# Kernel optimization log

Measured on AMD Instinct MI355X. Metric: run time of the kernel, lower is better.

The kernel has to match this reference:

```python
import jax, jax.numpy as jnp
import numpy as np

POS_MARGIN = 0.1
NEG_MARGIN = 1.4
LOG_SCALE = 24.0
MAX_POINTS = 256

N_FULL = 50000
M_C = 2048
N_C = 2048
D_FEAT = 256
K_CORR = 4096
N_BACK = 30000


def setup_inputs() -> dict:
    key = jax.random.key(0)
    ks = jax.random.split(key, 12)
    ref_feats = jax.random.normal(ks[4], (M_C, D_FEAT), jnp.float32)
    src_feats = jax.random.normal(ks[5], (N_C, D_FEAT), jnp.float32)
    # features are assumed L2-normalized (pairwise_distance(..., normalized=True))
    ref_feats = ref_feats / jnp.linalg.norm(ref_feats, axis=-1, keepdims=True)
    src_feats = src_feats / jnp.linalg.norm(src_feats, axis=-1, keepdims=True)
    return {
        "ref_points": jax.random.normal(ks[0], (N_FULL, 3), jnp.float32),
        "src_points": jax.random.normal(ks[1], (N_FULL, 3), jnp.float32),
        "ref_points_c": jax.random.normal(ks[2], (M_C, 3), jnp.float32),
        "src_points_c": jax.random.normal(ks[3], (N_C, 3), jnp.float32),
        "ref_feats_c": ref_feats,
        "src_feats_c": src_feats,
        "gt_node_corr_indices": jax.random.randint(ks[6], (K_CORR, 2), 0, M_C, dtype=jnp.int64) if jax.config.jax_enable_x64 else jax.random.randint(ks[6], (K_CORR, 2), 0, M_C, dtype=jnp.int32),
        "gt_node_corr_overlaps": jax.random.uniform(ks[7], (K_CORR,), jnp.float32),
        "corr_sp_mask": jax.random.uniform(ks[8], (M_C + N_C,), jnp.float32),
        "ref_back_indices": jax.random.randint(ks[9], (N_BACK,), 0, N_FULL, dtype=jnp.int32),
        "src_back_indices": jax.random.randint(ks[10], (N_BACK,), 0, N_FULL, dtype=jnp.int32),
    }


def _nn_indices(full_points, corr_points):
    # argmin over squared euclidean distance == argmin over cdist(p=2)
    d = (jnp.sum(corr_points ** 2, axis=1)[:, None]
         + jnp.sum(full_points ** 2, axis=1)[None, :]
         - 2.0 * corr_points @ full_points.T)  # [k, N]
    return jnp.argmin(d, axis=1)


def _forward(ref_points, src_points, ref_points_c, src_points_c,
             ref_feats_c, src_feats_c, gt_node_corr_overlaps, corr_sp_mask,
             gt_node_corr_indices, ref_back_indices, src_back_indices):
    m = ref_feats_c.shape[0]
    n = src_feats_c.shape[0]

    idx_ref = _nn_indices(ref_points, ref_points_c)  # [m]
    idx_src = _nn_indices(src_points, src_points_c)  # [n]

    # mask_ref[i] True iff idx_ref[i] appears in ref_back_indices (set intersection semantics)
    mask_ref = jnp.any(idx_ref[:, None] == ref_back_indices[None, :], axis=1)
    mask_src = jnp.any(idx_src[:, None] == src_back_indices[None, :], axis=1)

    xi = gt_node_corr_indices[:, 0]
    yi = gt_node_corr_indices[:, 1]
    corr_gt = jnp.zeros((m, n), dtype=bool).at[xi, yi].set(True)
    corr_overlap = jnp.zeros((m, n), jnp.float32).at[xi, yi].set(gt_node_corr_overlaps)

    corr_gt = corr_gt & (mask_ref[:, None] & mask_src[None, :])
    gt_mask = jnp.concatenate([mask_ref, mask_src]).astype(jnp.float32)  # [m+n]

    # cap number of positives at MAX_POINTS by overlap score
    count = jnp.sum(corr_gt)
    score = jnp.where(corr_gt, corr_overlap, -1.0).reshape(-1)
    topv, topi = jax.lax.top_k(score, MAX_POINTS)
    capped = jnp.zeros((m * n,), dtype=bool).at[topi].set(topv > -0.5).reshape(m, n)
    corr_gt = jnp.where(count > MAX_POINTS, capped, corr_gt)

    var_mask = 1.0 - corr_sp_mask  # [m+n]

    # NLLLaplace
    feat_sq = jnp.maximum(2.0 - 2.0 * (ref_feats_c @ src_feats_c.T), 0.0)
    feat_dists = jnp.sqrt(feat_sq)  # [m, n]
    laplace_mask = var_mask[:m][:, None] * var_mask[m:m + n][None, :]
    feat_dists = jnp.exp(0.5 * laplace_mask) * feat_dists

    not_pos = (~corr_gt).astype(jnp.float32)
    not_neg = corr_gt.astype(jnp.float32)
    pos_w = jax.lax.stop_gradient(
        jnp.maximum(feat_dists - 100000.0 * not_pos - POS_MARGIN, 0.0))
    neg_w = jax.lax.stop_gradient(
        jnp.maximum(NEG_MARGIN - (feat_dists + 100000.0 * not_neg), 0.0))

    lp = LOG_SCALE * (feat_dists - POS_MARGIN) * pos_w
    ln = LOG_SCALE * (NEG_MARGIN - feat_dists) * neg_w
    loss_row = jax.nn.softplus(jax.nn.logsumexp(lp, axis=-1) + jax.nn.logsumexp(ln, axis=-1)) / LOG_SCALE
    loss_col = jax.nn.softplus(jax.nn.logsumexp(lp, axis=-2) + jax.nn.logsumexp(ln, axis=-2)) / LOG_SCALE
    loss1 = (jnp.mean(loss_row) + jnp.mean(loss_col)) / 2.0
    loss2 = jnp.mean(jnp.abs(var_mask - gt_mask))
    loss = loss1 + loss2
    return loss, loss1, loss2


def reference(ref_points, src_points, ref_points_c, src_points_c,
              ref_feats_c, src_feats_c, gt_node_corr_indices,
              gt_node_corr_overlaps, corr_sp_mask,
              ref_back_indices, src_back_indices):
    return _forward(ref_points, src_points, ref_points_c, src_points_c,
                    ref_feats_c, src_feats_c, gt_node_corr_overlaps, corr_sp_mask,
                    gt_node_corr_indices, ref_back_indices, src_back_indices)
```

## Files before the change

kernel.cpp:

```cpp
#include <hip/hip_runtime.h>
#include <math.h>

using u8  = unsigned char;
using u32 = unsigned int;
using u64 = unsigned long long;

typedef short short8 __attribute__((ext_vector_type(8)));
typedef float f32x4  __attribute__((ext_vector_type(4)));

#define MC 2048
#define NC 2048
#define DF 256
#define NFULL 50000
#define NBACK 30000
#define KCORR 4096
#define MAXPTS 256
#define NN_CHUNK 196
#define BM_WORDS_I 1568

constexpr size_t OFF_ROWP = 0;
constexpr size_t OFF_COLP = (size_t)2 * 1024 * 1024;
constexpr size_t OFF_GTB  = (size_t)3 * 1024 * 1024;
constexpr size_t OFF_NN   = OFF_GTB + (size_t)512 * 1024;
constexpr size_t OFF_CAND = OFF_NN + 4096 * 8;
constexpr size_t OFF_ACC  = OFF_CAND + 4096 * 8;
constexpr size_t OFF_CNT  = OFF_ACC + 256;
constexpr size_t OFF_BM   = OFF_CNT + 256;
constexpr size_t OFF_HASH = OFF_BM + 3200 * 4;

__global__ __launch_bounds__(256) void k_init(uint4* __restrict__ gtb4, u64* __restrict__ nn,
                                              float* __restrict__ acc, u64* __restrict__ hash,
                                              u32* __restrict__ cnt, u32* __restrict__ bm) {
    int e = blockIdx.x * 256 + threadIdx.x;
    gtb4[e] = make_uint4(0u, 0u, 0u, 0u);
    if (e < 8192) hash[e] = 0ull;
    if (e < 4096) nn[e] = ~0ull;
    if (e < 2 * BM_WORDS_I) bm[e] = 0u;
    if (e < 8) acc[e] = 0.f;
    if (e < 2) cnt[e] = 0u;
}

__global__ __launch_bounds__(256) void k_nn(
        const float* __restrict__ fr, const float* __restrict__ fs,
        const float* __restrict__ cr, const float* __restrict__ cs,
        const int* __restrict__ rbi, const int* __restrict__ sbi,
        u32* __restrict__ bm, u64* __restrict__ nn) {
    const int side = blockIdx.y;
    const float* full = side ? fs : fr;
    const float* corr = side ? cs : cr;
    const int ib = blockIdx.x & 1, ch = blockIdx.x >> 1;
    const int t = threadIdx.x;

    int gb = side * 512 + blockIdx.x;
    if (gb < 235) {
        int e = gb * 256 + t;
        if (e < 2 * NBACK) {
            int s2 = e < NBACK ? 0 : 1;
            int v = s2 ? sbi[e - NBACK] : rbi[e];
            atomicOr(&bm[s2 * BM_WORDS_I + (v >> 5)], 1u << (v & 31));
        }
    }

    __shared__ float4 s4[NN_CHUNK];
    const int j0 = ch * NN_CHUNK;
    for (int e = t; e < NN_CHUNK; e += 256) {
        int j = j0 + e;
        float4 v;
        if (j < NFULL) {
            float x = full[j*3], y = full[j*3+1], z = full[j*3+2];
            v = make_float4(x, y, z, x*x + y*y + z*z);
        } else {
            v = make_float4(0.f, 0.f, 0.f, 3.0e38f);
        }
        s4[e] = v;
    }

    float ax[4], ay[4], az[4], bd[4];
    int bg[4];
    #pragma unroll
    for (int q = 0; q < 4; ++q) {
        int i = ib * 1024 + q * 256 + t;
        float cx = corr[i*3], cy = corr[i*3+1], cz = corr[i*3+2];
        ax[q] = -2.f*cx; ay[q] = -2.f*cy; az[q] = -2.f*cz;
        bd[q] = 3.4e38f; bg[q] = 0;
    }
    __syncthreads();

    #pragma unroll 2
    for (int g = 0; g < 49; ++g) {
        float4 p0 = s4[g*4+0], p1 = s4[g*4+1], p2 = s4[g*4+2], p3 = s4[g*4+3];
        #pragma unroll
        for (int q = 0; q < 4; ++q) {
            float d0 = fmaf(ax[q], p0.x, fmaf(ay[q], p0.y, fmaf(az[q], p0.z, p0.w)));
            float d1 = fmaf(ax[q], p1.x, fmaf(ay[q], p1.y, fmaf(az[q], p1.z, p1.w)));
            float d2 = fmaf(ax[q], p2.x, fmaf(ay[q], p2.y, fmaf(az[q], p2.z, p2.w)));
            float d3 = fmaf(ax[q], p3.x, fmaf(ay[q], p3.y, fmaf(az[q], p3.z, p3.w)));
            float gm = fminf(fminf(d0, d1), fminf(d2, d3));
            bool win = gm < bd[q];
            bd[q] = fminf(bd[q], gm);
            bg[q] = win ? g : bg[q];
        }
    }

    #pragma unroll
    for (int q = 0; q < 4; ++q) {
        int base = bg[q] * 4;
        u32 bj = (u32)(j0 + base);
        bool found = false;
        #pragma unroll
        for (int u = 0; u < 4; ++u) {
            float4 p = s4[base + u];
            float d = fmaf(ax[q], p.x, fmaf(ay[q], p.y, fmaf(az[q], p.z, p.w)));
            if (!found && d == bd[q]) { bj = (u32)(j0 + base + u); found = true; }
        }
        int i = ib * 1024 + q * 256 + t;
        float cn = 0.25f * fmaf(ax[q], ax[q], fmaf(ay[q], ay[q], az[q]*az[q]));
        float bf = bd[q] + cn;
        u32 db = __float_as_uint(bf);
        db = (db & 0x80000000u) ? ~db : (db | 0x80000000u);
        atomicMin(&nn[side * 2048 + i], ((u64)db << 32) | bj);
    }
}

__device__ __forceinline__ u32 mask_of(const u64* nn, const u32* bm, int idx, int side) {
    u32 j = (u32)(nn[idx] & 0xFFFFFFFFull);
    return (bm[side * BM_WORDS_I + (j >> 5)] >> (j & 31)) & 1u;
}

__global__ __launch_bounds__(256) void k_msc(
        const u64* __restrict__ nn, const u32* __restrict__ bm,
        const float* __restrict__ spm, const int* __restrict__ gti,
        u32* __restrict__ gtb, u64* __restrict__ hash, float* __restrict__ acc) {
    const int t = threadIdx.x;
    if (blockIdx.x == 0) {
        __shared__ float red[4];
        float c = 0.f;
        for (int e = t; e < 4096; e += 256)
            c += fabsf((1.f - spm[e]) - (float)mask_of(nn, bm, e, e >> 11));
        for (int o = 32; o; o >>= 1) c += __shfl_xor(c, o);
        if ((t & 63) == 0) red[t >> 6] = c;
        __syncthreads();
        if (t == 0) acc[2] = red[0] + red[1] + red[2] + red[3];
    }

    int k = blockIdx.x * 256 + t;
    int xi = gti[2*k], yi = gti[2*k+1];
    u32 cell = (u32)(xi * 2048 + yi);
    u32 masked = mask_of(nn, bm, xi, 0) & mask_of(nn, bm, 2048 + yi, 1);
    if (masked) atomicOr(&gtb[xi * 64 + (yi >> 5)], 1u << (yi & 31));
    u64 val = ((u64)(cell + 1) << 13) | ((u64)masked << 12) | (u32)k;
    u32 h = (cell * 2654435761u) >> 19;
    while (true) {
        u64 cur = hash[h];
        if (cur == 0ull) cur = atomicCAS(&hash[h], 0ull, val);
        if (cur == 0ull) break;
        if ((cur >> 13) == (u64)(cell + 1)) { atomicMax(&hash[h], val); break; }
        h = (h + 1) & 8191;
    }
}

__global__ void k_scat2(const u64* __restrict__ hash, const float* __restrict__ gtv,
                        u64* __restrict__ cand, u32* __restrict__ cnt) {
    int e = blockIdx.x * 256 + threadIdx.x;
    u64 s = hash[e];
    if (s == 0ull) return;
    if (!((s >> 12) & 1ull)) return;
    u32 cell = (u32)(s >> 13) - 1u;
    u32 k = (u32)(s & 0xFFFull);
    u32 vb = __float_as_uint(gtv[k]);
    u32 idx = atomicAdd(cnt, 1u);
    cand[idx] = ((u64)vb << 22) | (u32)(0x3FFFFF - cell);
}

__global__ __launch_bounds__(256) void k_top(const u64* __restrict__ cand,
                                             const u32* __restrict__ cnt,
                                             u32* __restrict__ gtb) {
    const int n = (int)cnt[0];
    if (n <= MAXPTS) return;
    if (blockIdx.x * 256 >= n) return;
    __shared__ u64 keys[4096];
    const int t = threadIdx.x;
    for (int e = t; e < n; e += 256) keys[e] = cand[e];
    __syncthreads();
    int c = blockIdx.x * 256 + t;
    if (c >= n) return;
    u64 me = keys[c];
    int rank = 0;
    #pragma unroll 4
    for (int j = 0; j < n; ++j) rank += (keys[j] > me);
    if (rank >= MAXPTS) {
        u32 cell = 0x3FFFFFu - (u32)(me & 0x3FFFFFull);
        int row = cell >> 11, col = cell & 2047;
        atomicAnd(&gtb[row * 64 + (col >> 5)], ~(1u << (col & 31)));
    }
}

__device__ __forceinline__ void circle_terms(float d, bool g, float& lp, float& ln) {
    if (g) { float a = d - 0.1f; lp = a > 0.f ? 24.f*a*a : 0.f; ln = 0.f; }
    else   { float b = 1.4f - d; ln = b > 0.f ? 24.f*b*b : 0.f; lp = 0.f; }
}

__device__ __forceinline__ float softplus_(float x) {
    return fmaxf(x, 0.f) + log1pf(expf(-fabsf(x)));
}

__global__ __launch_bounds__(256) void k_gemm(
        const float* __restrict__ A, const float* __restrict__ B,
        const float* __restrict__ spm, const u32* __restrict__ gtb,
        float4* __restrict__ rowp, float4* __restrict__ colp) {
    __shared__ __align__(16) short As[16384];
    __shared__ __align__(16) short Bs[8192];
    __shared__ u32 gtw[256];
    const int t = threadIdx.x;
    const int l = t & 63, wid = t >> 6;
    const int wm = wid >> 1, wn = wid & 1;
    const int i0 = blockIdx.y * 128, j0 = blockIdx.x * 64;

    gtw[t] = gtb[(size_t)(i0 + (t >> 1)) * 64 + (j0 >> 5) + (t & 1)];

    f32x4 acc[4][2] = {};

    for (int ks = 0; ks < 2; ++ks) {
        __syncthreads();
        #pragma unroll
        for (int it = 0; it < 12; ++it) {
            int sl = it * 256 + t;
            int c = sl & 63, q = c >> 4, r15 = c & 15;
            const float* src;
            short* dst;
            int kf;
            if (it < 8) {
                int frag = sl >> 6;
                kf = frag & 3;
                int row = (frag >> 2) * 16 + r15;
                src = A + (size_t)(i0 + row) * 256;
                dst = &As[sl * 8];
            } else {
                int sl2 = sl - 2048;
                int frag = sl2 >> 6;
                kf = frag & 3;
                int row = (frag >> 2) * 16 + r15;
                src = B + (size_t)(j0 + row) * 256;
                dst = &Bs[sl2 * 8];
            }
            int col = ks * 128 + kf * 32 + q * 8;
            float4 v0 = *(const float4*)(src + col);
            float4 v1 = *(const float4*)(src + col + 4);
            u32 w0 = __builtin_amdgcn_perm(__float_as_uint(v0.y), __float_as_uint(v0.x), 0x07060302u);
            u32 w1 = __builtin_amdgcn_perm(__float_as_uint(v0.w), __float_as_uint(v0.z), 0x07060302u);
            u32 w2 = __builtin_amdgcn_perm(__float_as_uint(v1.y), __float_as_uint(v1.x), 0x07060302u);
            u32 w3 = __builtin_amdgcn_perm(__float_as_uint(v1.w), __float_as_uint(v1.z), 0x07060302u);
            *(uint4*)dst = make_uint4(w0, w1, w2, w3);
        }
        __syncthreads();

        #pragma unroll
        for (int kf = 0; kf < 4; ++kf) {
            short8 a[4], b[2];
            #pragma unroll
            for (int mi = 0; mi < 4; ++mi)
                a[mi] = *(const short8*)&As[(((wm*4 + mi)*4 + kf) << 9) + l*8];
            #pragma unroll
            for (int ni = 0; ni < 2; ++ni)
                b[ni] = *(const short8*)&Bs[(((wn*2 + ni)*4 + kf) << 9) + l*8];
            #pragma unroll
            for (int mi = 0; mi < 4; ++mi)
                #pragma unroll
                for (int ni = 0; ni < 2; ++ni)
                    acc[mi][ni] = __builtin_amdgcn_mfma_f32_16x16x32_bf16(
                        a[mi], b[ni], acc[mi][ni], 0, 0, 0);
        }
    }

    const int cq = l >> 4, cr = l & 15;
    const int rows0 = i0 + wm * 64, cols0 = j0 + wn * 32;

    float vmj[2];
    #pragma unroll
    for (int ni = 0; ni < 2; ++ni) vmj[ni] = 1.f - spm[2048 + cols0 + ni*16 + cr];
    float vmi[4][4];
    #pragma unroll
    for (int mi = 0; mi < 4; ++mi)
        #pragma unroll
        for (int rr = 0; rr < 4; ++rr)
            vmi[mi][rr] = 1.f - spm[rows0 + mi*16 + cq*4 + rr];

    u32 gmask = 0;
    #pragma unroll
    for (int mi = 0; mi < 4; ++mi)
        #pragma unroll
        for (int rr = 0; rr < 4; ++rr) {
            u32 w = gtw[(wm*64 + mi*16 + cq*4 + rr) * 2 + wn];
            #pragma unroll
            for (int ni = 0; ni < 2; ++ni)
                if ((w >> (ni*16 + cr)) & 1u) gmask |= 1u << (mi*8 + ni*4 + rr);
        }
    #pragma unroll
    for (int mi = 0; mi < 4; ++mi)
        #pragma unroll
        for (int ni = 0; ni < 2; ++ni)
            #pragma unroll
            for (int rr = 0; rr < 4; ++rr) {
                float s  = acc[mi][ni][rr];
                float fs = fmaxf(2.f - 2.f*s, 0.f);
                acc[mi][ni][rr] = sqrtf(fs) * expf(0.5f * vmi[mi][rr] * vmj[ni]);
            }

    const int jt2 = blockIdx.x * 2 + wn;
    const int it2 = blockIdx.y * 2 + wm;

    #pragma unroll
    for (int mi = 0; mi < 4; ++mi)
        #pragma unroll
        for (int rr = 0; rr < 4; ++rr) {
            float lp0, ln0, lp1, ln1;
            circle_terms(acc[mi][0][rr], (gmask >> (mi*8 + rr)) & 1, lp0, ln0);
            circle_terms(acc[mi][1][rr], (gmask >> (mi*8 + 4 + rr)) & 1, lp1, ln1);
            float mp = fmaxf(lp0, lp1), mn = fmaxf(ln0, ln1);
            #pragma unroll
            for (int o = 1; o < 16; o <<= 1) {
                mp = fmaxf(mp, __shfl_xor(mp, o));
                mn = fmaxf(mn, __shfl_xor(mn, o));
            }
            float sp = expf(lp0 - mp) + expf(lp1 - mp);
            float sn = expf(ln0 - mn) + expf(ln1 - mn);
            #pragma unroll
            for (int o = 1; o < 16; o <<= 1) {
                sp += __shfl_xor(sp, o);
                sn += __shfl_xor(sn, o);
            }
            if (cr == mi*4 + rr) {
                int row = rows0 + mi*16 + cq*4 + rr;
                rowp[(size_t)jt2 * 2048 + row] = make_float4(mp, sp, mn, sn);
            }
        }

    #pragma unroll
    for (int ni = 0; ni < 2; ++ni) {
        float lp[16], ln[16];
        #pragma unroll
        for (int mi = 0; mi < 4; ++mi)
            #pragma unroll
            for (int rr = 0; rr < 4; ++rr)
                circle_terms(acc[mi][ni][rr], (gmask >> (mi*8 + ni*4 + rr)) & 1,
                             lp[mi*4+rr], ln[mi*4+rr]);
        float mp = lp[0], mn = ln[0];
        #pragma unroll
        for (int e = 1; e < 16; ++e) { mp = fmaxf(mp, lp[e]); mn = fmaxf(mn, ln[e]); }
        #pragma unroll
        for (int o = 16; o < 64; o <<= 1) {
            mp = fmaxf(mp, __shfl_xor(mp, o));
            mn = fmaxf(mn, __shfl_xor(mn, o));
        }
        float sp = 0.f, sn = 0.f;
        #pragma unroll
        for (int e = 0; e < 16; ++e) { sp += expf(lp[e] - mp); sn += expf(ln[e] - mn); }
        #pragma unroll
        for (int o = 16; o < 64; o <<= 1) {
            sp += __shfl_xor(sp, o);
            sn += __shfl_xor(sn, o);
        }
        if (cq == 0) {
            int col = cols0 + ni*16 + cr;
            colp[(size_t)it2 * 2048 + col] = make_float4(mp, sp, mn, sn);
        }
    }
}

__global__ __launch_bounds__(256) void k_merge(const float4* __restrict__ rowp,
                                               const float4* __restrict__ colp,
                                               float* __restrict__ acc,
                                               u32* __restrict__ cnt,
                                               float* __restrict__ out) {
    const int t = threadIdx.x;
    const int bx = blockIdx.x;
    float Mp = -1e30f, Sp = 0.f, Mn = -1e30f, Sn = 0.f;
    if (bx < 8) {
        int row = bx * 256 + t;
        for (int jt = 0; jt < 64; ++jt) {
            float4 p = rowp[(size_t)jt * 2048 + row];
            float nm = fmaxf(Mp, p.x); Sp = Sp*expf(Mp-nm) + p.y*expf(p.x-nm); Mp = nm;
            nm = fmaxf(Mn, p.z); Sn = Sn*expf(Mn-nm) + p.w*expf(p.z-nm); Mn = nm;
        }
    } else {
        int col = (bx - 8) * 256 + t;
        for (int it = 0; it < 32; ++it) {
            float4 p = colp[(size_t)it * 2048 + col];
            float nm = fmaxf(Mp, p.x); Sp = Sp*expf(Mp-nm) + p.y*expf(p.x-nm); Mp = nm;
            nm = fmaxf(Mn, p.z); Sn = Sn*expf(Mn-nm) + p.w*expf(p.z-nm); Mn = nm;
        }
    }
    float x = (Mp + logf(Sp)) + (Mn + logf(Sn));
    float lv = softplus_(x) * (1.f / 24.f);
    for (int o = 32; o; o >>= 1) lv += __shfl_xor(lv, o);
    __shared__ float wsum[4];
    __shared__ u32 tic;
    if ((t & 63) == 0) wsum[t >> 6] = lv;
    __syncthreads();
    if (t == 0) {
        atomicAdd(&acc[bx < 8 ? 0 : 1], wsum[0] + wsum[1] + wsum[2] + wsum[3]);
        __threadfence();
        tic = atomicAdd(&cnt[1], 1u);
    }
    __syncthreads();
    if (t == 0 && tic == 15u) {
        __threadfence();
        float a0 = atomicAdd(&acc[0], 0.f);
        float a1 = atomicAdd(&acc[1], 0.f);
        float a2 = atomicAdd(&acc[2], 0.f);
        float l1 = (a0 + a1) * (0.5f / 2048.f);
        float l2 = a2 * (1.f / 4096.f);
        out[0] = l1 + l2; out[1] = l1; out[2] = l2;
    }
}

extern "C" void kernel_launch(void* const* d_in, const int* in_sizes, int n_in,
                              void* d_out, int out_size, void* d_ws, size_t ws_size,
                              hipStream_t stream) {
    (void)in_sizes; (void)n_in; (void)out_size; (void)ws_size;
    const float* ref_points = (const float*)d_in[0];
    const float* src_points = (const float*)d_in[1];
    const float* ref_c      = (const float*)d_in[2];
    const float* src_c      = (const float*)d_in[3];
    const float* ref_f      = (const float*)d_in[4];
    const float* src_f      = (const float*)d_in[5];
    const int*   gti        = (const int*)d_in[6];
    const float* gtv        = (const float*)d_in[7];
    const float* spm        = (const float*)d_in[8];
    const int*   rbi        = (const int*)d_in[9];
    const int*   sbi        = (const int*)d_in[10];

    char* ws = (char*)d_ws;
    float4* rowp = (float4*)(ws + OFF_ROWP);
    float4* colp = (float4*)(ws + OFF_COLP);
    u32*   gtb  = (u32*)  (ws + OFF_GTB);
    u64*   nn   = (u64*)  (ws + OFF_NN);
    u64*   cand = (u64*)  (ws + OFF_CAND);
    float* acc  = (float*)(ws + OFF_ACC);
    u32*   cnt  = (u32*)  (ws + OFF_CNT);
    u32*   bm   = (u32*)  (ws + OFF_BM);
    u64*   hash = (u64*)  (ws + OFF_HASH);

    k_init <<<128, 256, 0, stream>>>((uint4*)gtb, nn, acc, hash, cnt, bm);
    k_nn   <<<dim3(512, 2), 256, 0, stream>>>(ref_points, src_points, ref_c, src_c,
                                              rbi, sbi, bm, nn);
    k_msc  <<<16, 256, 0, stream>>>(nn, bm, spm, gti, gtb, hash, acc);
    k_scat2<<<32, 256, 0, stream>>>(hash, gtv, cand, cnt);
    k_top  <<<16, 256, 0, stream>>>(cand, cnt, gtb);
    k_gemm <<<dim3(32, 16), 256, 0, stream>>>(ref_f, src_f, spm, gtb, rowp, colp);
    k_merge<<<16, 256, 0, stream>>>(rowp, colp, acc, cnt, (float*)d_out);
}
```

Measured before the change: 118.2 us.

## Fuse candidate scatter and top-k into k_msc via last-block ticket; SoA packed-FMA NN

Two kernel launches (k_scat2, k_top) are folded into k_msc. The last block to finish, found with an atomic ticket counter, compacts the hash table into shared memory and does the rank-based top-k pruning itself. The NN search layout changes from one float4 per point to SoA float4 groups, so distances can be computed with two-wide packed FMAs. This removes launch overhead and the global candidate buffer. In exchange, the top-k runs serially in one block (one pass of 256 threads instead of 16 blocks) and shared-memory usage in k_msc grows.

```diff
diff --git a/kernel.cpp b/kernel.cpp
--- a/kernel.cpp
+++ b/kernel.cpp
@@ -7,6 +7,7 @@
 
 typedef short short8 __attribute__((ext_vector_type(8)));
 typedef float f32x4  __attribute__((ext_vector_type(4)));
+typedef float f32x2  __attribute__((ext_vector_type(2)));
 
 #define MC 2048
 #define NC 2048
@@ -22,8 +23,7 @@
 constexpr size_t OFF_COLP = (size_t)2 * 1024 * 1024;
 constexpr size_t OFF_GTB  = (size_t)3 * 1024 * 1024;
 constexpr size_t OFF_NN   = OFF_GTB + (size_t)512 * 1024;
-constexpr size_t OFF_CAND = OFF_NN + 4096 * 8;
-constexpr size_t OFF_ACC  = OFF_CAND + 4096 * 8;
+constexpr size_t OFF_ACC  = OFF_NN + 4096 * 8;
 constexpr size_t OFF_CNT  = OFF_ACC + 256;
 constexpr size_t OFF_BM   = OFF_CNT + 256;
 constexpr size_t OFF_HASH = OFF_BM + 3200 * 4;
@@ -37,7 +37,7 @@
     if (e < 4096) nn[e] = ~0ull;
     if (e < 2 * BM_WORDS_I) bm[e] = 0u;
     if (e < 8) acc[e] = 0.f;
-    if (e < 2) cnt[e] = 0u;
+    if (e < 4) cnt[e] = 0u;
 }
 
 __global__ __launch_bounds__(256) void k_nn(
@@ -61,18 +61,26 @@
         }
     }
 
-    __shared__ float4 s4[NN_CHUNK];
+    __shared__ float4 sx4[49], sy4[49], sz4[49], sw4[49];
     const int j0 = ch * NN_CHUNK;
-    for (int e = t; e < NN_CHUNK; e += 256) {
-        int j = j0 + e;
-        float4 v;
-        if (j < NFULL) {
-            float x = full[j*3], y = full[j*3+1], z = full[j*3+2];
-            v = make_float4(x, y, z, x*x + y*y + z*z);
-        } else {
-            v = make_float4(0.f, 0.f, 0.f, 3.0e38f);
-        }
-        s4[e] = v;
+    if (t < 49) {
+        int b4 = j0 + t * 4;
+        float xx[4], yy[4], zz[4], ww[4];
+        #pragma unroll
+        for (int u = 0; u < 4; ++u) {
+            int j = b4 + u;
+            if (j < NFULL) {
+                float x = full[j*3], y = full[j*3+1], z = full[j*3+2];
+                xx[u] = x; yy[u] = y; zz[u] = z;
+                ww[u] = fmaf(x, x, fmaf(y, y, z*z));
+            } else {
+                xx[u] = 0.f; yy[u] = 0.f; zz[u] = 0.f; ww[u] = 3.0e38f;
+            }
+        }
+        sx4[t] = make_float4(xx[0], xx[1], xx[2], xx[3]);
+        sy4[t] = make_float4(yy[0], yy[1], yy[2], yy[3]);
+        sz4[t] = make_float4(zz[0], zz[1], zz[2], zz[3]);
+        sw4[t] = make_float4(ww[0], ww[1], ww[2], ww[3]);
     }
 
     float ax[4], ay[4], az[4], bd[4];
@@ -88,14 +96,22 @@
 
     #pragma unroll 2
     for (int g = 0; g < 49; ++g) {
-        float4 p0 = s4[g*4+0], p1 = s4[g*4+1], p2 = s4[g*4+2], p3 = s4[g*4+3];
+        float4 X = sx4[g], Y = sy4[g], Z = sz4[g], W = sw4[g];
+        f32x2 xlo = {X.x, X.y}, xhi = {X.z, X.w};
+        f32x2 ylo = {Y.x, Y.y}, yhi = {Y.z, Y.w};
+        f32x2 zlo = {Z.x, Z.y}, zhi = {Z.z, Z.w};
+        f32x2 wlo = {W.x, W.y}, whi = {W.z, W.w};
         #pragma unroll
         for (int q = 0; q < 4; ++q) {
-            float d0 = fmaf(ax[q], p0.x, fmaf(ay[q], p0.y, fmaf(az[q], p0.z, p0.w)));
-            float d1 = fmaf(ax[q], p1.x, fmaf(ay[q], p1.y, fmaf(az[q], p1.z, p1.w)));
-            float d2 = fmaf(ax[q], p2.x, fmaf(ay[q], p2.y, fmaf(az[q], p2.z, p2.w)));
-            float d3 = fmaf(ax[q], p3.x, fmaf(ay[q], p3.y, fmaf(az[q], p3.z, p3.w)));
-            float gm = fminf(fminf(d0, d1), fminf(d2, d3));
+            f32x2 aq = {ax[q], ax[q]}, bq = {ay[q], ay[q]}, cq2 = {az[q], az[q]};
+            f32x2 dlo = __builtin_elementwise_fma(aq, xlo,
+                          __builtin_elementwise_fma(bq, ylo,
+                            __builtin_elementwise_fma(cq2, zlo, wlo)));
+            f32x2 dhi = __builtin_elementwise_fma(aq, xhi,
+                          __builtin_elementwise_fma(bq, yhi,
+                            __builtin_elementwise_fma(cq2, zhi, whi)));
+            f32x2 m2 = __builtin_elementwise_min(dlo, dhi);
+            float gm = fminf(m2.x, m2.y);
             bool win = gm < bd[q];
             bd[q] = fminf(bd[q], gm);
             bg[q] = win ? g : bg[q];
@@ -104,14 +120,25 @@
 
     #pragma unroll
     for (int q = 0; q < 4; ++q) {
-        int base = bg[q] * 4;
-        u32 bj = (u32)(j0 + base);
+        int gsel = bg[q];
+        float4 X = sx4[gsel], Y = sy4[gsel], Z = sz4[gsel], W = sw4[gsel];
+        f32x2 xlo = {X.x, X.y}, xhi = {X.z, X.w};
+        f32x2 ylo = {Y.x, Y.y}, yhi = {Y.z, Y.w};
+        f32x2 zlo = {Z.x, Z.y}, zhi = {Z.z, Z.w};
+        f32x2 wlo = {W.x, W.y}, whi = {W.z, W.w};
+        f32x2 aq = {ax[q], ax[q]}, bq = {ay[q], ay[q]}, cq2 = {az[q], az[q]};
+        f32x2 dlo = __builtin_elementwise_fma(aq, xlo,
+                      __builtin_elementwise_fma(bq, ylo,
+                        __builtin_elementwise_fma(cq2, zlo, wlo)));
+        f32x2 dhi = __builtin_elementwise_fma(aq, xhi,
+                      __builtin_elementwise_fma(bq, yhi,
+                        __builtin_elementwise_fma(cq2, zhi, whi)));
+        float dv[4] = {dlo.x, dlo.y, dhi.x, dhi.y};
+        u32 bj = (u32)(j0 + gsel * 4);
         bool found = false;
         #pragma unroll
         for (int u = 0; u < 4; ++u) {
-            float4 p = s4[base + u];
-            float d = fmaf(ax[q], p.x, fmaf(ay[q], p.y, fmaf(az[q], p.z, p.w)));
-            if (!found && d == bd[q]) { bj = (u32)(j0 + base + u); found = true; }
+            if (!found && dv[u] == bd[q]) { bj = (u32)(j0 + gsel*4 + u); found = true; }
         }
         int i = ib * 1024 + q * 256 + t;
         float cn = 0.25f * fmaf(ax[q], ax[q], fmaf(ay[q], ay[q], az[q]*az[q]));
@@ -130,7 +157,9 @@
 __global__ __launch_bounds__(256) void k_msc(
         const u64* __restrict__ nn, const u32* __restrict__ bm,
         const float* __restrict__ spm, const int* __restrict__ gti,
-        u32* __restrict__ gtb, u64* __restrict__ hash, float* __restrict__ acc) {
+        const float* __restrict__ gtv,
+        u32* __restrict__ gtb, u64* __restrict__ hash,
+        u32* __restrict__ cnt, float* __restrict__ acc) {
     const int t = threadIdx.x;
     if (blockIdx.x == 0) {
         __shared__ float red[4];
@@ -157,41 +186,40 @@
         if ((cur >> 13) == (u64)(cell + 1)) { atomicMax(&hash[h], val); break; }
         h = (h + 1) & 8191;
     }
-}
-
-__global__ void k_scat2(const u64* __restrict__ hash, const float* __restrict__ gtv,
-                        u64* __restrict__ cand, u32* __restrict__ cnt) {
-    int e = blockIdx.x * 256 + threadIdx.x;
-    u64 s = hash[e];
-    if (s == 0ull) return;
-    if (!((s >> 12) & 1ull)) return;
-    u32 cell = (u32)(s >> 13) - 1u;
-    u32 k = (u32)(s & 0xFFFull);
-    u32 vb = __float_as_uint(gtv[k]);
-    u32 idx = atomicAdd(cnt, 1u);
-    cand[idx] = ((u64)vb << 22) | (u32)(0x3FFFFF - cell);
-}
-
-__global__ __launch_bounds__(256) void k_top(const u64* __restrict__ cand,
-                                             const u32* __restrict__ cnt,
-                                             u32* __restrict__ gtb) {
-    const int n = (int)cnt[0];
+
+    __shared__ u32 s_tic;
+    __threadfence();
+    __syncthreads();
+    if (t == 0) s_tic = atomicAdd(&cnt[2], 1u);
+    __syncthreads();
+    if (s_tic != 15u) return;
+
+    __shared__ u64 keys[4096];
+    __shared__ int s_n;
+    if (t == 0) s_n = 0;
+    __syncthreads();
+    for (int e = t; e < 8192; e += 256) {
+        u64 s = __hip_atomic_load(&hash[e], __ATOMIC_RELAXED, __HIP_MEMORY_SCOPE_AGENT);
+        if (s == 0ull) continue;
+        if (!((s >> 12) & 1ull)) continue;
+        u32 cl = (u32)(s >> 13) - 1u;
+        u32 kk = (u32)(s & 0xFFFull);
+        u32 vb = __float_as_uint(gtv[kk]);
+        int idx = atomicAdd(&s_n, 1);
+        keys[idx] = ((u64)vb << 22) | (u32)(0x3FFFFF - cl);
+    }
+    __syncthreads();
+    const int n = s_n;
     if (n <= MAXPTS) return;
-    if (blockIdx.x * 256 >= n) return;
-    __shared__ u64 keys[4096];
-    const int t = threadIdx.x;
-    for (int e = t; e < n; e += 256) keys[e] = cand[e];
-    __syncthreads();
-    int c = blockIdx.x * 256 + t;
-    if (c >= n) return;
-    u64 me = keys[c];
-    int rank = 0;
-    #pragma unroll 4
-    for (int j = 0; j < n; ++j) rank += (keys[j] > me);
-    if (rank >= MAXPTS) {
-        u32 cell = 0x3FFFFFu - (u32)(me & 0x3FFFFFull);
-        int row = cell >> 11, col = cell & 2047;
-        atomicAnd(&gtb[row * 64 + (col >> 5)], ~(1u << (col & 31)));
+    for (int c = t; c < n; c += 256) {
+        u64 me = keys[c];
+        int rank = 0;
+        for (int j = 0; j < n; ++j) rank += (keys[j] > me);
+        if (rank >= MAXPTS) {
+            u32 cl = 0x3FFFFFu - (u32)(me & 0x3FFFFFull);
+            int row = cl >> 11, col = cl & 2047;
+            atomicAnd(&gtb[row * 64 + (col >> 5)], ~(1u << (col & 31)));
+        }
     }
 }
 
@@ -435,7 +463,6 @@
     float4* colp = (float4*)(ws + OFF_COLP);
     u32*   gtb  = (u32*)  (ws + OFF_GTB);
     u64*   nn   = (u64*)  (ws + OFF_NN);
-    u64*   cand = (u64*)  (ws + OFF_CAND);
     float* acc  = (float*)(ws + OFF_ACC);
     u32*   cnt  = (u32*)  (ws + OFF_CNT);
     u32*   bm   = (u32*)  (ws + OFF_BM);
@@ -444,9 +471,7 @@
     k_init <<<128, 256, 0, stream>>>((uint4*)gtb, nn, acc, hash, cnt, bm);
     k_nn   <<<dim3(512, 2), 256, 0, stream>>>(ref_points, src_points, ref_c, src_c,
                                               rbi, sbi, bm, nn);
-    k_msc  <<<16, 256, 0, stream>>>(nn, bm, spm, gti, gtb, hash, acc);
-    k_scat2<<<32, 256, 0, stream>>>(hash, gtv, cand, cnt);
-    k_top  <<<16, 256, 0, stream>>>(cand, cnt, gtb);
+    k_msc  <<<16, 256, 0, stream>>>(nn, bm, spm, gti, gtv, gtb, hash, cnt, acc);
     k_gemm <<<dim3(32, 16), 256, 0, stream>>>(ref_f, src_f, spm, gtb, rowp, colp);
     k_merge<<<16, 256, 0, stream>>>(rowp, colp, acc, cnt, (float*)d_out);
 }
```

After: 158.8 us. 34.3% more time.
